# Kernel optimization log

Measured on AMD Instinct MI355X. Metric: run time of the kernel, lower is better.

## Reference

```python
import jax, jax.numpy as jnp
import numpy as np

N_E = 1024
E_DIM = 512
LEGACY_CLUSTER = 0.2
LEGACY_ENERGY = 0.2


def setup_inputs() -> dict:
    key = jax.random.key(0)
    k1, k2 = jax.random.split(key)
    B, T = 64, 512
    key_soft = jax.random.normal(k1, (B, T, E_DIM), dtype=jnp.float32)
    zero_ts_mask = jnp.zeros((B,), dtype=bool)
    # nn.Embedding(1+n_e, e_dim) initialized uniform(-1/n_e, 1/n_e)
    emb_weight = jax.random.uniform(k2, (N_E + 1, E_DIM), dtype=jnp.float32,
                                    minval=-1.0 / N_E, maxval=1.0 / N_E)
    return {"key_soft": key_soft, "zero_ts_mask": zero_ts_mask, "emb_weight": emb_weight}


def _compute_indices(d3, zero_ts_mask, n_e):
    # d3: [B, T, n_e+1] squared distances (treated as constants: torch.no_grad)
    ind0 = jnp.clip(jnp.argmin(d3[:, 0, :], axis=1), 0, n_e - 1)
    ind0 = jnp.where(zero_ts_mask, 0, ind0)

    def step(ind, d_t):
        # d_t: [B, n_e+1]; neighbor-constrained argmin: stay at ind or move to ind+1
        d_here = jnp.take_along_axis(d_t, ind[:, None], axis=1)[:, 0]
        ind_next = jnp.clip(ind + 1, 0, n_e - 1)
        d_next = jnp.take_along_axis(d_t, ind_next[:, None], axis=1)[:, 0]
        new_ind = jnp.where(d_here <= d_next, ind, ind_next)
        return new_ind, new_ind

    d_rest = jnp.swapaxes(d3[:, 1:, :], 0, 1)  # [T-1, B, n_e+1] time-major
    _, inds_rest = jax.lax.scan(step, ind0, d_rest)
    return jnp.concatenate([ind0[:, None], jnp.swapaxes(inds_rest, 0, 1)], axis=1)  # [B, T]


def reference(key_soft, zero_ts_mask, emb_weight):
    sg = jax.lax.stop_gradient
    B, T, e_dim = key_soft.shape
    n_e = emb_weight.shape[0] - 1
    ksf = key_soft.reshape(-1, e_dim)  # [B*T, e_dim]
    # squared euclidean distances to all 1+n_e codes: [B*T, n_e+1]
    d = (jnp.sum(ksf ** 2, axis=1, keepdims=True)
         + jnp.sum(emb_weight ** 2, axis=1)
         - 2.0 * jnp.einsum('bd,nd->bn', ksf, emb_weight))
    min_indices = jnp.argmin(d, axis=1)  # [B*T]
    d3 = d.reshape(B, T, n_e + 1)
    encoding_indices = _compute_indices(sg(d3), zero_ts_mask, n_e)  # [B, T]

    key_hard_here = emb_weight[encoding_indices]        # [B, T, e_dim]
    key_hard_next = emb_weight[encoding_indices + 1]    # [B, T, e_dim]
    key_min = emb_weight[min_indices].reshape(B, T, e_dim)

    key_em_here = (jnp.sum((sg(key_soft) - key_hard_here) ** 2, axis=-1)
                   + jnp.sum((key_soft - sg(key_hard_here)) ** 2, axis=-1) * LEGACY_ENERGY)
    key_em_next = (jnp.sum((sg(key_soft) - key_hard_next) ** 2, axis=-1)
                   + jnp.sum((key_soft - sg(key_hard_next)) ** 2, axis=-1) * LEGACY_ENERGY)
    key_energy_mat = key_em_next - key_em_here  # [B, T]

    ind_change = (encoding_indices[:, 1:] - encoding_indices[:, :-1]).astype(bool)
    key_energy_change = (key_energy_mat[:, 1:] - key_energy_mat[:, :-1]) * jnp.where(ind_change, 0.0, 1.0)
    eps = 1e-06 / n_e
    loss_key_energy_descent = jnp.maximum(key_energy_change + eps, 0.0).mean()

    loss_min_indices = (jnp.sum((sg(key_soft) - key_min) ** 2, axis=-1)
                        + jnp.sum((key_soft - sg(key_min)) ** 2, axis=-1) * LEGACY_CLUSTER)
    reg_persist_mat = jnp.exp(-key_em_next)
    e_normal_mat = jnp.where(key_em_here > loss_min_indices - eps,
                             key_em_here - loss_min_indices + eps,
                             key_em_here) + reg_persist_mat
    e_abnormal_mat = key_em_next + jnp.exp(-key_em_here)

    key_hard = key_soft + sg(key_hard_here - key_soft)  # straight-through
    v = jnp.max(jnp.max(encoding_indices, axis=1) - jnp.min(encoding_indices, axis=1))
    return (key_hard, encoding_indices, v, loss_key_energy_descent,
            key_energy_mat, e_normal_mat, e_abnormal_mat)
```

## Files before the change

### kernel.cpp

```cpp
#include <hip/hip_runtime.h>
#include <math.h>

typedef unsigned char u8;
typedef unsigned short u16;
typedef unsigned int u32;
typedef __attribute__((ext_vector_type(8))) short bf16x8;
typedef __attribute__((ext_vector_type(4))) float f32x4;

#define O1 16777216
#define O2 16809984
#define O3 16809985
#define O4 16809986
#define O5 16842754
#define O6 16875522

#define W_COLSQ 0
#define W_MINV  4352
#define W_MINI  2101504
#define W_SF    4198656
#define W_SL    6426880
#define W_BITS  8524032
#define W_MIDX  12718336
#define W_ENC   12849408
#define W_V     12980480
#define W_P5    12980736
#define W_EH    13000704
#define W_EL    14050304

__device__ __forceinline__ u32 cvt_pk(float lo, float hi) {
  u32 r;
  asm volatile("v_cvt_pk_bf16_f32 %0, %1, %2" : "=v"(r) : "v"(lo), "v"(hi));
  return r;
}
__device__ __forceinline__ float asf(u32 u) { return __uint_as_float(u); }

__device__ __forceinline__ void gload_lds16(const void* g, void* l) {
  __builtin_amdgcn_global_load_lds(
      (const __attribute__((address_space(1))) unsigned int*)g,
      (__attribute__((address_space(3))) unsigned int*)l, 16, 0, 0);
}

__global__ __launch_bounds__(256) void k0_colsq(const float* __restrict__ emb,
                                                float* __restrict__ colsq,
                                                u32* __restrict__ emb_hi,
                                                u32* __restrict__ emb_lo) {
  int w = threadIdx.x >> 6, lane = threadIdx.x & 63;
  int c = blockIdx.x * 4 + w;
  if (c >= 1025) return;
  const float4* e4 = (const float4*)(emb + (size_t)c * 512);
  float4 a = e4[lane * 2], b = e4[lane * 2 + 1];
  float p = a.x * a.x + a.y * a.y + a.z * a.z + a.w * a.w
          + b.x * b.x + b.y * b.y + b.z * b.z + b.w * b.w;
  #pragma unroll
  for (int off = 32; off; off >>= 1) p += __shfl_xor(p, off);
  if (lane == 0) colsq[c] = p;
  u32 h0 = cvt_pk(a.x, a.y), h1 = cvt_pk(a.z, a.w);
  u32 h2 = cvt_pk(b.x, b.y), h3 = cvt_pk(b.z, b.w);
  float l0 = a.x - asf(h0 << 16), l1 = a.y - asf(h0 & 0xFFFF0000u);
  float l2 = a.z - asf(h1 << 16), l3 = a.w - asf(h1 & 0xFFFF0000u);
  float l4 = b.x - asf(h2 << 16), l5 = b.y - asf(h2 & 0xFFFF0000u);
  float l6 = b.z - asf(h3 << 16), l7 = b.w - asf(h3 & 0xFFFF0000u);
  uint4 hv; hv.x = h0; hv.y = h1; hv.z = h2; hv.w = h3;
  uint4 lv; lv.x = cvt_pk(l0, l1); lv.y = cvt_pk(l2, l3);
  lv.z = cvt_pk(l4, l5); lv.w = cvt_pk(l6, l7);
  ((uint4*)emb_hi)[c * 64 + lane] = hv;
  ((uint4*)emb_lo)[c * 64 + lane] = lv;
}

__global__ __launch_bounds__(256) void k1_gemm(const float* __restrict__ ksf,
                                               const u32* __restrict__ emb_hi,
                                               const u32* __restrict__ emb_lo,
                                               const float* __restrict__ colsq,
                                               float* __restrict__ minv, int* __restrict__ mini,
                                               float* __restrict__ sF, float* __restrict__ sL,
                                               u8* __restrict__ bits) {
  __shared__ float smemf[16384];
  char* smc = (char*)smemf;
  const int tid = threadIdx.x, bid = blockIdx.x;
  const int g = bid >> 6;
  const int cbk = (bid >> 3) & 7;
  const int rb = g * 8 + (bid & 7);
  const int r0 = rb * 128, c0 = cbk * 128;
  const int lane = tid & 63, w = tid >> 6;
  const int wr = w >> 1, wc = w & 1;
  const int q = lane >> 4, li = lane & 15;

  int offS[4], baseA[4];
  #pragma unroll
  for (int i = 0; i < 4; i++) {
    int p = tid + (i << 8);
    int row = p >> 3, q8 = p & 7;
    offS[i] = row * 64 + ((q8 * 8) ^ (((row >> 1) & 3) << 4));
    baseA[i] = (r0 + row) * 128 + q8;
  }
  const int rowj0 = w * 32 + (lane >> 2), rowj1 = rowj0 + 16;
  const int qb = lane & 3;
  const int offB0 = (c0 + rowj0) * 1024 + ((qb ^ ((rowj0 >> 1) & 3)) << 4);
  const int offB1 = (c0 + rowj1) * 1024 + ((qb ^ ((rowj1 >> 1) & 3)) << 4);
  const char* ebh = (const char*)emb_hi;
  const char* ebl = (const char*)emb_lo;

  int foA[4], foB[4];
  #pragma unroll
  for (int m = 0; m < 4; m++) {
    int row = wr * 64 + m * 16 + li;
    foA[m] = row * 64 + ((q * 16) ^ (((row >> 1) & 3) << 4));
    int col = wc * 64 + m * 16 + li;
    foB[m] = col * 64 + ((q * 16) ^ (((col >> 1) & 3) << 4));
  }

  f32x4 acc[4][4];
  #pragma unroll
  for (int m = 0; m < 4; m++)
    #pragma unroll
    for (int n = 0; n < 4; n++) acc[m][n] = (f32x4){0.f, 0.f, 0.f, 0.f};

  const float4* A4 = (const float4*)ksf;
  float4 ra[4];

  auto stageB = [&](int bb, int t1) {
    int ko = t1 * 64;
    char* d0 = smc + bb + 16384 + w * 2048;
    gload_lds16(ebh + offB0 + ko, d0);
    gload_lds16(ebh + offB1 + ko, d0 + 1024);
    gload_lds16(ebl + offB0 + ko, d0 + 8192);
    gload_lds16(ebl + offB1 + ko, d0 + 9216);
  };
  auto stageA = [&](int bb) {
    #pragma unroll
    for (int i = 0; i < 4; i++) {
      float4 v = ra[i];
      u32 w0 = cvt_pk(v.x, v.y), w1 = cvt_pk(v.z, v.w);
      float lx = v.x - asf(w0 << 16);
      float ly = v.y - asf(w0 & 0xFFFF0000u);
      float lz = v.z - asf(w1 << 16);
      float lw = v.w - asf(w1 & 0xFFFF0000u);
      u32 m0 = cvt_pk(lx, ly), m1 = cvt_pk(lz, lw);
      uint2 hv; hv.x = w0; hv.y = w1;
      uint2 lv; lv.x = m0; lv.y = m1;
      *(uint2*)(smc + bb + offS[i]) = hv;
      *(uint2*)(smc + bb + 8192 + offS[i]) = lv;
    }
  };
  auto mfma_phase = [&](int bb) {
    bf16x8 fA[4], fB[4], fX[4];
    #pragma unroll
    for (int m = 0; m < 4; m++) fA[m] = *(const bf16x8*)(smc + bb + foA[m]);
    #pragma unroll
    for (int n = 0; n < 4; n++) fB[n] = *(const bf16x8*)(smc + bb + 16384 + foB[n]);
    #pragma unroll
    for (int m = 0; m < 4; m++)
      #pragma unroll
      for (int n = 0; n < 4; n++)
        acc[m][n] = __builtin_amdgcn_mfma_f32_16x16x32_bf16(fA[m], fB[n], acc[m][n], 0, 0, 0);
    #pragma unroll
    for (int n = 0; n < 4; n++) fX[n] = *(const bf16x8*)(smc + bb + 24576 + foB[n]);
    #pragma unroll
    for (int m = 0; m < 4; m++)
      #pragma unroll
      for (int n = 0; n < 4; n++)
        acc[m][n] = __builtin_amdgcn_mfma_f32_16x16x32_bf16(fA[m], fX[n], acc[m][n], 0, 0, 0);
    #pragma unroll
    for (int m = 0; m < 4; m++) fA[m] = *(const bf16x8*)(smc + bb + 8192 + foA[m]);
    #pragma unroll
    for (int m = 0; m < 4; m++)
      #pragma unroll
      for (int n = 0; n < 4; n++)
        acc[m][n] = __builtin_amdgcn_mfma_f32_16x16x32_bf16(fA[m], fB[n], acc[m][n], 0, 0, 0);
  };

  #pragma unroll
  for (int i = 0; i < 4; i++) ra[i] = A4[baseA[i]];
  stageB(0, 0);
  stageA(0);
  #pragma unroll
  for (int i = 0; i < 4; i++) ra[i] = A4[baseA[i] + 8];
  __syncthreads();

  #pragma unroll 1
  for (int tp = 0; tp < 8; tp++) {
    int t = tp * 2;
    {
      stageB(32768, t + 1);
      stageA(32768);
      if (t < 14) {
        #pragma unroll
        for (int i = 0; i < 4; i++) ra[i] = A4[baseA[i] + (t + 2) * 8];
      }
      __builtin_amdgcn_s_setprio(1);
      mfma_phase(0);
      __builtin_amdgcn_s_setprio(0);
      __syncthreads();
    }
    {
      int t1 = t + 1;
      if (t1 < 15) {
        stageB(0, t1 + 1);
        stageA(0);
        if (t1 < 14) {
          #pragma unroll
          for (int i = 0; i < 4; i++) ra[i] = A4[baseA[i] + (t1 + 2) * 8];
        }
      }
      __builtin_amdgcn_s_setprio(1);
      mfma_phase(32768);
      __builtin_amdgcn_s_setprio(0);
      __syncthreads();
    }
  }

  float cs4[4];
  #pragma unroll
  for (int n = 0; n < 4; n++) cs4[n] = colsq[c0 + wc * 64 + n * 16 + li];
  const int ct = tid & 15, rt = tid >> 4;
  for (int h = 0; h < 2; h++) {
    __syncthreads();
    if (wr == h) {
      #pragma unroll
      for (int m = 0; m < 4; m++) {
        int rl = m * 16 + q * 4;
        #pragma unroll
        for (int n = 0; n < 4; n++) {
          int cl = wc * 64 + n * 16 + li;
          #pragma unroll
          for (int r = 0; r < 4; r++)
            smemf[(rl + r) * 132 + cl] = fmaf(acc[m][n][r], -2.0f, cs4[n]);
        }
      }
    }
    __syncthreads();
    #pragma unroll
    for (int j = 0; j < 4; j++) {
      int rl = rt * 4 + j;
      int rowg = r0 + h * 64 + rl;
      const float* sp = &smemf[rl * 132 + ct * 8];
      float4 sa = *(const float4*)sp, sb = *(const float4*)(sp + 4);
      float s[8] = {sa.x, sa.y, sa.z, sa.w, sb.x, sb.y, sb.z, sb.w};
      float sn0 = __shfl_down(s[0], 1, 16);
      u32 bv = 0;
      #pragma unroll
      for (int i = 0; i < 7; i++) bv |= (s[i] <= s[i + 1]) ? (1u << i) : 0u;
      bv |= (s[7] <= sn0) ? 0x80u : 0u;
      bits[rowg * 128 + cbk * 16 + ct] = (u8)bv;
      int cbase = c0 + ct * 8;
      float mv = s[0]; int mi = cbase;
      #pragma unroll
      for (int i = 1; i < 8; i++) if (s[i] < mv) { mv = s[i]; mi = cbase + i; }
      #pragma unroll
      for (int d = 4; d >= 1; d >>= 1) {
        float ov = __shfl_xor(mv, d, 8);
        int oi = __shfl_xor(mi, d, 8);
        if (ov < mv || (ov == mv && oi < mi)) { mv = ov; mi = oi; }
      }
      int sb64 = cbk * 2 + (ct >> 3);
      if ((ct & 7) == 0) {
        minv[rowg * 16 + sb64] = mv;
        mini[rowg * 16 + sb64] = mi;
        sF[rowg * 17 + sb64] = s[0];
      }
      if ((ct & 7) == 7) sL[rowg * 16 + sb64] = s[7];
    }
  }
}

__global__ __launch_bounds__(256) void k1b_col1024(const float* __restrict__ ksf,
                                                   const float* __restrict__ emb,
                                                   const float* __restrict__ colsq,
                                                   float* __restrict__ sF) {
  int wid = threadIdx.x >> 6, lane = threadIdx.x & 63;
  int row = blockIdx.x * 4 + wid;
  const float4* ks4 = (const float4*)(ksf + (size_t)row * 512);
  const float4* e4 = (const float4*)(emb + (size_t)1024 * 512);
  float4 a = ks4[lane * 2], b = ks4[lane * 2 + 1];
  float4 ea = e4[lane * 2], eb = e4[lane * 2 + 1];
  float p = a.x * ea.x + a.y * ea.y + a.z * ea.z + a.w * ea.w
          + b.x * eb.x + b.y * eb.y + b.z * eb.z + b.w * eb.w;
  #pragma unroll
  for (int off = 32; off; off >>= 1) p += __shfl_xor(p, off);
  if (lane == 0) sF[row * 17 + 16] = fmaf(p, -2.0f, colsq[1024]);
}

__global__ __launch_bounds__(256) void k2_combine(const float* __restrict__ minv,
                                                  const int* __restrict__ mini,
                                                  const float* __restrict__ sF,
                                                  const float* __restrict__ sL,
                                                  u8* __restrict__ bits,
                                                  int* __restrict__ midx, int* __restrict__ vslot) {
  int row = blockIdx.x * 256 + threadIdx.x;
  if (blockIdx.x == 0 && threadIdx.x == 0) *vslot = 0;
  float bv = minv[row * 16];
  int bi = mini[row * 16];
  #pragma unroll
  for (int cb = 1; cb < 16; cb++) {
    float v = minv[row * 16 + cb];
    int ii = mini[row * 16 + cb];
    if (v < bv) { bv = v; bi = ii; }
  }
  float s1024 = sF[row * 17 + 16];
  if (s1024 < bv) { bv = s1024; bi = 1024; }
  midx[row] = bi;
  #pragma unroll
  for (int cb = 0; cb < 16; cb++) {
    float nb = (cb < 15) ? sF[row * 17 + cb + 1] : s1024;
    u8 bit = (sL[row * 16 + cb] <= nb) ? (u8)0x80 : (u8)0;
    int a = row * 128 + cb * 8 + 7;
    bits[a] = (u8)((bits[a] & 0x7F) | bit);
  }
}

__global__ __launch_bounds__(256) void k3_scan(const u8* __restrict__ bits,
                                               const int* __restrict__ midx,
                                               const u8* __restrict__ mask,
                                               int* __restrict__ enc, int* __restrict__ vslot) {
  __shared__ u32 bl[256 * 32];
  __shared__ int el[512];
  int b = blockIdx.x, tid = threadIdx.x, lane = tid & 63;
  const u32* bw = (const u32*)bits;
  for (int phase = 0; phase < 2; phase++) {
    int t0 = 1 + phase * 256;
    int nt = phase ? 255 : 256;
    __syncthreads();
    for (int ww = tid; ww < nt * 32; ww += 256)
      bl[ww] = bw[(size_t)(b * 512 + t0) * 32 + ww];
    __syncthreads();
    if (tid < 64) {
      int ind;
      if (phase == 0) {
        int mi = midx[b * 512];
        ind = mi < 1023 ? mi : 1023;
        if (ind < 0) ind = 0;
        if (mask[b]) ind = 0;
        if (lane == 0) el[0] = ind;
      } else {
        ind = el[256];
      }
      int done = 0;
      while (done < nt) {
        int W = nt - done; if (W > 64) W = 64;
        int i0 = ind;
        int p = i0 + lane;
        u32 mlo = 0xFFFFFFFFu, mhi = 0xFFFFFFFFu;
        if (p < 1023) {
          int base = done * 32 + (p >> 5);
          int sh = p & 31;
          mlo = 0; mhi = 0;
          #pragma unroll
          for (int s = 0; s < 32; s++)
            mlo |= ((bl[base + s * 32] >> sh) & 1u) << s;
          #pragma unroll
          for (int s = 0; s < 32; s++)
            mhi |= ((bl[base + (s + 32) * 32] >> sh) & 1u) << s;
        }
        int rel = 0, myel = 0;
        #pragma unroll
        for (int s = 0; s < 64; s++) {
          u32 wv = (s < 32) ? __builtin_amdgcn_readlane(mlo, rel)
                            : __builtin_amdgcn_readlane(mhi, rel);
          rel += 1 - (int)((wv >> (s & 31)) & 1u);
          if (lane == s) myel = i0 + rel;
        }
        if (lane < W) el[t0 + done + lane] = myel;
        ind = (int)__builtin_amdgcn_readlane((u32)myel, (u32)(W - 1));
        done += W;
      }
    }
  }
  __syncthreads();
  for (int t = tid; t < 512; t += 256) enc[b * 512 + t] = el[t];
  if (tid == 0) atomicMax(vslot, el[511] - el[0]);
}

__global__ __launch_bounds__(256) void k4_energy(const float* __restrict__ ksf,
                                                 const float* __restrict__ emb,
                                                 const int* __restrict__ enc_a,
                                                 const int* __restrict__ midx,
                                                 float* __restrict__ out) {
  int wid = threadIdx.x >> 6, lane = threadIdx.x & 63;
  int row = blockIdx.x * 4 + wid;
  int eh = enc_a[row];
  int mi = midx[row];
  eh = (eh < 0) ? 0 : (eh > 1023 ? 1023 : eh);
  mi = (mi < 0) ? 0 : (mi > 1024 ? 1024 : mi);
  const float4* ks4 = (const float4*)(ksf + (size_t)row * 512);
  const float4* h4 = (const float4*)(emb + (size_t)eh * 512);
  const float4* n4 = (const float4*)(emb + (size_t)(eh + 1) * 512);
  const float4* m4 = (const float4*)(emb + (size_t)mi * 512);
  float ph = 0.f, pn = 0.f, pm = 0.f;
  float4 kh[2];
  #pragma unroll
  for (int u = 0; u < 2; u++) {
    float4 k = ks4[lane * 2 + u], h = h4[lane * 2 + u], n = n4[lane * 2 + u], m = m4[lane * 2 + u];
    float d;
    d = k.x - h.x; ph = fmaf(d, d, ph);
    d = k.y - h.y; ph = fmaf(d, d, ph);
    d = k.z - h.z; ph = fmaf(d, d, ph);
    d = k.w - h.w; ph = fmaf(d, d, ph);
    d = k.x - n.x; pn = fmaf(d, d, pn);
    d = k.y - n.y; pn = fmaf(d, d, pn);
    d = k.z - n.z; pn = fmaf(d, d, pn);
    d = k.w - n.w; pn = fmaf(d, d, pn);
    d = k.x - m.x; pm = fmaf(d, d, pm);
    d = k.y - m.y; pm = fmaf(d, d, pm);
    d = k.z - m.z; pm = fmaf(d, d, pm);
    d = k.w - m.w; pm = fmaf(d, d, pm);
    kh[u].x = k.x + (h.x - k.x);
    kh[u].y = k.y + (h.y - k.y);
    kh[u].z = k.z + (h.z - k.z);
    kh[u].w = k.w + (h.w - k.w);
  }
  #pragma unroll
  for (int off = 32; off; off >>= 1) {
    ph += __shfl_xor(ph, off);
    pn += __shfl_xor(pn, off);
    pm += __shfl_xor(pm, off);
  }
  float4* o0 = (float4*)out;
  o0[(size_t)row * 128 + lane * 2] = kh[0];
  o0[(size_t)row * 128 + lane * 2 + 1] = kh[1];
  if (lane == 0) {
    const float epsN = 9.765625e-10f;
    float kemh = ph + ph * 0.2f;
    float kemn = pn + pn * 0.2f;
    float lmin = pm + pm * 0.2f;
    float lminu = fminf(lmin, kemh);
    out[O1 + row] = (float)eh;
    out[O4 + row] = kemn - kemh;
    float env = (kemh > lminu - epsN) ? ((kemh - lminu) + epsN) : kemh;
    out[O5 + row] = env + expf(-kemn);
    out[O6 + row] = kemn + expf(-kemh);
  }
}

__global__ __launch_bounds__(256) void k5a_part(const float* __restrict__ kem,
                                                const int* __restrict__ enc,
                                                float* __restrict__ partial) {
  __shared__ float red[256];
  int tid = threadIdx.x;
  int i = blockIdx.x * 256 + tid;
  const float epsN = 9.765625e-10f;
  float p = 0.f;
  if (i & 511) {
    float diff = kem[i] - kem[i - 1];
    if (enc[i] != enc[i - 1]) diff = 0.f;
    float v = diff + epsN;
    p = (v > 0.f) ? v : 0.f;
  }
  red[tid] = p;
  __syncthreads();
  #pragma unroll
  for (int s = 128; s; s >>= 1) {
    if (tid < s) red[tid] += red[tid + s];
    __syncthreads();
  }
  if (tid == 0) partial[blockIdx.x] = red[0];
}

__global__ __launch_bounds__(64) void k5b_final(const float* __restrict__ partial,
                                                const int* __restrict__ vslot,
                                                float* __restrict__ out) {
  int lane = threadIdx.x;
  float p = partial[lane] + partial[lane + 64];
  #pragma unroll
  for (int off = 32; off; off >>= 1) p += __shfl_xor(p, off);
  if (lane == 0) {
    out[O3] = p / 32704.0f;
    out[O2] = (float)(*vslot);
  }
}

extern "C" void kernel_launch(void* const* d_in, const int* in_sizes, int n_in,
                              void* d_out, int out_size, void* d_ws, size_t ws_size,
                              hipStream_t stream) {
  const float* ksf = (const float*)d_in[0];
  const u8* mask = (const u8*)d_in[1];
  const float* emb = (const float*)d_in[2];
  float* out = (float*)d_out;
  char* ws = (char*)d_ws;
  float* colsq = (float*)(ws + W_COLSQ);
  float* minv = (float*)(ws + W_MINV);
  int* mini = (int*)(ws + W_MINI);
  float* sF = (float*)(ws + W_SF);
  float* sL = (float*)(ws + W_SL);
  u8* bits = (u8*)(ws + W_BITS);
  int* midx = (int*)(ws + W_MIDX);
  int* enc = (int*)(ws + W_ENC);
  int* vslot = (int*)(ws + W_V);
  u32* emb_hi = (u32*)(ws + W_EH);
  u32* emb_lo = (u32*)(ws + W_EL);
  float* part5 = (float*)(ws + W_P5);

  hipLaunchKernelGGL(k0_colsq, dim3(257), dim3(256), 0, stream, emb, colsq, emb_hi, emb_lo);
  hipLaunchKernelGGL(k1_gemm, dim3(2048), dim3(256), 0, stream, ksf, emb_hi, emb_lo, colsq,
                     minv, mini, sF, sL, bits);
  hipLaunchKernelGGL(k1b_col1024, dim3(8192), dim3(256), 0, stream, ksf, emb, colsq, sF);
  hipLaunchKernelGGL(k2_combine, dim3(128), dim3(256), 0, stream, minv, mini, sF, sL,
                     bits, midx, vslot);
  hipLaunchKernelGGL(k3_scan, dim3(64), dim3(256), 0, stream, bits, midx, mask, enc, vslot);
  hipLaunchKernelGGL(k4_energy, dim3(8192), dim3(256), 0, stream, ksf, emb, enc, midx, out);
  hipLaunchKernelGGL(k5a_part, dim3(128), dim3(256), 0, stream, out + O4, enc, part5);
  hipLaunchKernelGGL(k5b_final, dim3(1), dim3(64), 0, stream, part5, vslot, out);
}
```

Before: 193.0 us.

## Load codebook B fragments directly from global into registers, shrink LDS for occupancy

Codebook hi/lo bf16 fragments are no longer staged into LDS through global_load_lds. Each wave now reads its own B fragments straight from global (L2-resident) memory into registers right before the MFMA phase. This halves the shared-memory footprint, and the launch bounds now request 3 blocks per CU to raise occupancy. The cost is that B loads are issued without prefetch and are duplicated across the two row-waves, so global latency sits directly ahead of the MFMAs.

```diff
diff --git a/kernel.cpp b/kernel.cpp
--- a/kernel.cpp
+++ b/kernel.cpp
@@ -33,12 +33,6 @@
   return r;
 }
 __device__ __forceinline__ float asf(u32 u) { return __uint_as_float(u); }
-
-__device__ __forceinline__ void gload_lds16(const void* g, void* l) {
-  __builtin_amdgcn_global_load_lds(
-      (const __attribute__((address_space(1))) unsigned int*)g,
-      (__attribute__((address_space(3))) unsigned int*)l, 16, 0, 0);
-}
 
 __global__ __launch_bounds__(256) void k0_colsq(const float* __restrict__ emb,
                                                 float* __restrict__ colsq,
@@ -67,14 +61,14 @@
   ((uint4*)emb_lo)[c * 64 + lane] = lv;
 }
 
-__global__ __launch_bounds__(256) void k1_gemm(const float* __restrict__ ksf,
-                                               const u32* __restrict__ emb_hi,
-                                               const u32* __restrict__ emb_lo,
-                                               const float* __restrict__ colsq,
-                                               float* __restrict__ minv, int* __restrict__ mini,
-                                               float* __restrict__ sF, float* __restrict__ sL,
-                                               u8* __restrict__ bits) {
-  __shared__ float smemf[16384];
+__global__ __launch_bounds__(256, 3) void k1_gemm(const float* __restrict__ ksf,
+                                                  const u32* __restrict__ emb_hi,
+                                                  const u32* __restrict__ emb_lo,
+                                                  const float* __restrict__ colsq,
+                                                  float* __restrict__ minv, int* __restrict__ mini,
+                                                  float* __restrict__ sF, float* __restrict__ sL,
+                                                  u8* __restrict__ bits) {
+  __shared__ float smemf[8448];
   char* smc = (char*)smemf;
   const int tid = threadIdx.x, bid = blockIdx.x;
   const int g = bid >> 6;
@@ -93,20 +87,20 @@
     offS[i] = row * 64 + ((q8 * 8) ^ (((row >> 1) & 3) << 4));
     baseA[i] = (r0 + row) * 128 + q8;
   }
-  const int rowj0 = w * 32 + (lane >> 2), rowj1 = rowj0 + 16;
-  const int qb = lane & 3;
-  const int offB0 = (c0 + rowj0) * 1024 + ((qb ^ ((rowj0 >> 1) & 3)) << 4);
-  const int offB1 = (c0 + rowj1) * 1024 + ((qb ^ ((rowj1 >> 1) & 3)) << 4);
+  int baseB[4];
+  #pragma unroll
+  for (int n = 0; n < 4; n++) {
+    int col = c0 + wc * 64 + n * 16 + li;
+    baseB[n] = col * 1024 + q * 16;
+  }
   const char* ebh = (const char*)emb_hi;
   const char* ebl = (const char*)emb_lo;
 
-  int foA[4], foB[4];
+  int foA[4];
   #pragma unroll
   for (int m = 0; m < 4; m++) {
     int row = wr * 64 + m * 16 + li;
     foA[m] = row * 64 + ((q * 16) ^ (((row >> 1) & 3) << 4));
-    int col = wc * 64 + m * 16 + li;
-    foB[m] = col * 64 + ((q * 16) ^ (((col >> 1) & 3) << 4));
   }
 
   f32x4 acc[4][4];
@@ -118,14 +112,6 @@
   const float4* A4 = (const float4*)ksf;
   float4 ra[4];
 
-  auto stageB = [&](int bb, int t1) {
-    int ko = t1 * 64;
-    char* d0 = smc + bb + 16384 + w * 2048;
-    gload_lds16(ebh + offB0 + ko, d0);
-    gload_lds16(ebh + offB1 + ko, d0 + 1024);
-    gload_lds16(ebl + offB0 + ko, d0 + 8192);
-    gload_lds16(ebl + offB1 + ko, d0 + 9216);
-  };
   auto stageA = [&](int bb) {
     #pragma unroll
     for (int i = 0; i < 4; i++) {
@@ -142,36 +128,31 @@
       *(uint2*)(smc + bb + 8192 + offS[i]) = lv;
     }
   };
-  auto mfma_phase = [&](int bb) {
-    bf16x8 fA[4], fB[4], fX[4];
+  auto mfma_phase = [&](int bb, const bf16x8* fB, const bf16x8* fX) {
+    bf16x8 fA[4], fL[4];
     #pragma unroll
     for (int m = 0; m < 4; m++) fA[m] = *(const bf16x8*)(smc + bb + foA[m]);
-    #pragma unroll
-    for (int n = 0; n < 4; n++) fB[n] = *(const bf16x8*)(smc + bb + 16384 + foB[n]);
     #pragma unroll
     for (int m = 0; m < 4; m++)
       #pragma unroll
       for (int n = 0; n < 4; n++)
         acc[m][n] = __builtin_amdgcn_mfma_f32_16x16x32_bf16(fA[m], fB[n], acc[m][n], 0, 0, 0);
     #pragma unroll
-    for (int n = 0; n < 4; n++) fX[n] = *(const bf16x8*)(smc + bb + 24576 + foB[n]);
-    #pragma unroll
     for (int m = 0; m < 4; m++)
       #pragma unroll
       for (int n = 0; n < 4; n++)
         acc[m][n] = __builtin_amdgcn_mfma_f32_16x16x32_bf16(fA[m], fX[n], acc[m][n], 0, 0, 0);
     #pragma unroll
-    for (int m = 0; m < 4; m++) fA[m] = *(const bf16x8*)(smc + bb + 8192 + foA[m]);
+    for (int m = 0; m < 4; m++) fL[m] = *(const bf16x8*)(smc + bb + 8192 + foA[m]);
     #pragma unroll
     for (int m = 0; m < 4; m++)
       #pragma unroll
       for (int n = 0; n < 4; n++)
-        acc[m][n] = __builtin_amdgcn_mfma_f32_16x16x32_bf16(fA[m], fB[n], acc[m][n], 0, 0, 0);
+        acc[m][n] = __builtin_amdgcn_mfma_f32_16x16x32_bf16(fL[m], fB[n], acc[m][n], 0, 0, 0);
   };
 
   #pragma unroll
   for (int i = 0; i < 4; i++) ra[i] = A4[baseA[i]];
-  stageB(0, 0);
   stageA(0);
   #pragma unroll
   for (int i = 0; i < 4; i++) ra[i] = A4[baseA[i] + 8];
@@ -181,21 +162,31 @@
   for (int tp = 0; tp < 8; tp++) {
     int t = tp * 2;
     {
-      stageB(32768, t + 1);
-      stageA(32768);
+      bf16x8 fB[4], fX[4];
+      #pragma unroll
+      for (int n = 0; n < 4; n++) {
+        fB[n] = *(const bf16x8*)(ebh + baseB[n] + t * 64);
+        fX[n] = *(const bf16x8*)(ebl + baseB[n] + t * 64);
+      }
+      stageA(16384);
       if (t < 14) {
         #pragma unroll
         for (int i = 0; i < 4; i++) ra[i] = A4[baseA[i] + (t + 2) * 8];
       }
       __builtin_amdgcn_s_setprio(1);
-      mfma_phase(0);
+      mfma_phase(0, fB, fX);
       __builtin_amdgcn_s_setprio(0);
       __syncthreads();
     }
     {
       int t1 = t + 1;
+      bf16x8 fB[4], fX[4];
+      #pragma unroll
+      for (int n = 0; n < 4; n++) {
+        fB[n] = *(const bf16x8*)(ebh + baseB[n] + t1 * 64);
+        fX[n] = *(const bf16x8*)(ebl + baseB[n] + t1 * 64);
+      }
       if (t1 < 15) {
-        stageB(0, t1 + 1);
         stageA(0);
         if (t1 < 14) {
           #pragma unroll
@@ -203,7 +194,7 @@
         }
       }
       __builtin_amdgcn_s_setprio(1);
-      mfma_phase(32768);
+      mfma_phase(16384, fB, fX);
       __builtin_amdgcn_s_setprio(0);
       __syncthreads();
     }
```

Result: slower. 340.6 us (+76.4%).

## Load emb low-part fragments directly from global in MFMA-ready layout, shrink LDS

Applied to the files above, without the earlier changes.

The k0 kernel now writes the low-bf16 part of the embedding in a pre-swizzled layout that matches the MFMA B-fragment order. The GEMM kernel reads these fragments straight from global memory into registers instead of staging them through LDS. This cuts LDS usage from 64KB to 48KB per block, which may raise occupancy and reduce LDS traffic. In exchange, the MFMA phase now waits on global load latency, and the 1025th code row's low part is no longer written.

```diff
diff --git a/kernel.cpp b/kernel.cpp
--- a/kernel.cpp
+++ b/kernel.cpp
@@ -27,6 +27,8 @@
 #define W_EH    13000704
 #define W_EL    14050304
 
+#define BUFST 24576
+
 __device__ __forceinline__ u32 cvt_pk(float lo, float hi) {
   u32 r;
   asm volatile("v_cvt_pk_bf16_f32 %0, %1, %2" : "=v"(r) : "v"(lo), "v"(hi));
@@ -64,7 +66,11 @@
   uint4 lv; lv.x = cvt_pk(l0, l1); lv.y = cvt_pk(l2, l3);
   lv.z = cvt_pk(l4, l5); lv.w = cvt_pk(l6, l7);
   ((uint4*)emb_hi)[c * 64 + lane] = hv;
-  ((uint4*)emb_lo)[c * 64 + lane] = lv;
+  if (c < 1024) {
+    int t = lane >> 2, qq = lane & 3;
+    int idx = (t * 16 + (c >> 6)) * 256 + ((c >> 4) & 3) * 64 + qq * 16 + (c & 15);
+    ((uint4*)emb_lo)[idx] = lv;
+  }
 }
 
 __global__ __launch_bounds__(256) void k1_gemm(const float* __restrict__ ksf,
@@ -74,7 +80,7 @@
                                                float* __restrict__ minv, int* __restrict__ mini,
                                                float* __restrict__ sF, float* __restrict__ sL,
                                                u8* __restrict__ bits) {
-  __shared__ float smemf[16384];
+  __shared__ float smemf[12288];
   char* smc = (char*)smemf;
   const int tid = threadIdx.x, bid = blockIdx.x;
   const int g = bid >> 6;
@@ -98,7 +104,8 @@
   const int offB0 = (c0 + rowj0) * 1024 + ((qb ^ ((rowj0 >> 1) & 3)) << 4);
   const int offB1 = (c0 + rowj1) * 1024 + ((qb ^ ((rowj1 >> 1) & 3)) << 4);
   const char* ebh = (const char*)emb_hi;
-  const char* ebl = (const char*)emb_lo;
+  const int baseL = (cbk * 2 + wc) * 256 + lane;
+  const uint4* Bl4 = (const uint4*)emb_lo;
 
   int foA[4], foB[4];
   #pragma unroll
@@ -123,8 +130,6 @@
     char* d0 = smc + bb + 16384 + w * 2048;
     gload_lds16(ebh + offB0 + ko, d0);
     gload_lds16(ebh + offB1 + ko, d0 + 1024);
-    gload_lds16(ebl + offB0 + ko, d0 + 8192);
-    gload_lds16(ebl + offB1 + ko, d0 + 9216);
   };
   auto stageA = [&](int bb) {
     #pragma unroll
@@ -142,8 +147,11 @@
       *(uint2*)(smc + bb + 8192 + offS[i]) = lv;
     }
   };
-  auto mfma_phase = [&](int bb) {
-    bf16x8 fA[4], fB[4], fX[4];
+  auto mfma_phase = [&](int bb, int t) {
+    bf16x8 gX[4];
+    #pragma unroll
+    for (int n = 0; n < 4; n++) gX[n] = *(const bf16x8*)&Bl4[t * 4096 + baseL + n * 64];
+    bf16x8 fA[4], fB[4], fL[4];
     #pragma unroll
     for (int m = 0; m < 4; m++) fA[m] = *(const bf16x8*)(smc + bb + foA[m]);
     #pragma unroll
@@ -154,19 +162,17 @@
       for (int n = 0; n < 4; n++)
         acc[m][n] = __builtin_amdgcn_mfma_f32_16x16x32_bf16(fA[m], fB[n], acc[m][n], 0, 0, 0);
     #pragma unroll
-    for (int n = 0; n < 4; n++) fX[n] = *(const bf16x8*)(smc + bb + 24576 + foB[n]);
-    #pragma unroll
     for (int m = 0; m < 4; m++)
       #pragma unroll
       for (int n = 0; n < 4; n++)
-        acc[m][n] = __builtin_amdgcn_mfma_f32_16x16x32_bf16(fA[m], fX[n], acc[m][n], 0, 0, 0);
-    #pragma unroll
-    for (int m = 0; m < 4; m++) fA[m] = *(const bf16x8*)(smc + bb + 8192 + foA[m]);
+        acc[m][n] = __builtin_amdgcn_mfma_f32_16x16x32_bf16(fA[m], gX[n], acc[m][n], 0, 0, 0);
+    #pragma unroll
+    for (int m = 0; m < 4; m++) fL[m] = *(const bf16x8*)(smc + bb + 8192 + foA[m]);
     #pragma unroll
     for (int m = 0; m < 4; m++)
       #pragma unroll
       for (int n = 0; n < 4; n++)
-        acc[m][n] = __builtin_amdgcn_mfma_f32_16x16x32_bf16(fA[m], fB[n], acc[m][n], 0, 0, 0);
+        acc[m][n] = __builtin_amdgcn_mfma_f32_16x16x32_bf16(fL[m], fB[n], acc[m][n], 0, 0, 0);
   };
 
   #pragma unroll
@@ -181,14 +187,14 @@
   for (int tp = 0; tp < 8; tp++) {
     int t = tp * 2;
     {
-      stageB(32768, t + 1);
-      stageA(32768);
+      stageB(BUFST, t + 1);
+      stageA(BUFST);
       if (t < 14) {
         #pragma unroll
         for (int i = 0; i < 4; i++) ra[i] = A4[baseA[i] + (t + 2) * 8];
       }
       __builtin_amdgcn_s_setprio(1);
-      mfma_phase(0);
+      mfma_phase(0, t);
       __builtin_amdgcn_s_setprio(0);
       __syncthreads();
     }
@@ -203,7 +209,7 @@
         }
       }
       __builtin_amdgcn_s_setprio(1);
-      mfma_phase(32768);
+      mfma_phase(BUFST, t1);
       __builtin_amdgcn_s_setprio(0);
       __syncthreads();
     }
```

Result: no change. 191.3 us (-0.9%).

## Fuse code-1024 distance column into GEMM blocks, drop separate kernel

Applied to the files above, without the earlier changes.

The extra distance column for code 1024 was computed by a separate kernel that re-read all of key_soft from global memory. Blocks handling the last column tile now hold the code-1024 row in registers and add extra split-bf16 MFMAs against the already-staged A fragments, writing sF column 16 directly. This removes one launch and a full pass over the 64MB input. In exchange, those blocks do extra MFMAs and register loads and become slightly imbalanced, and precision changes from fp32 FMA to a 3-term bf16 split.

```diff
diff --git a/kernel.cpp b/kernel.cpp
--- a/kernel.cpp
+++ b/kernel.cpp
@@ -81,6 +81,7 @@
   const int cbk = (bid >> 3) & 7;
   const int rb = g * 8 + (bid & 7);
   const int r0 = rb * 128, c0 = cbk * 128;
+  const bool cb7 = (cbk == 7);
   const int lane = tid & 63, w = tid >> 6;
   const int wr = w >> 1, wc = w & 1;
   const int q = lane >> 4, li = lane & 15;
@@ -99,6 +100,8 @@
   const int offB1 = (c0 + rowj1) * 1024 + ((qb ^ ((rowj1 >> 1) & 3)) << 4);
   const char* ebh = (const char*)emb_hi;
   const char* ebl = (const char*)emb_lo;
+  const char* e1024h = ebh + 1048576 + q * 16;
+  const char* e1024l = ebl + 1048576 + q * 16;
 
   int foA[4], foB[4];
   #pragma unroll
@@ -109,14 +112,18 @@
     foB[m] = col * 64 + ((q * 16) ^ (((col >> 1) & 3) << 4));
   }
 
-  f32x4 acc[4][4];
-  #pragma unroll
-  for (int m = 0; m < 4; m++)
+  f32x4 acc[4][4], acce[4];
+  #pragma unroll
+  for (int m = 0; m < 4; m++) {
+    acce[m] = (f32x4){0.f, 0.f, 0.f, 0.f};
     #pragma unroll
     for (int n = 0; n < 4; n++) acc[m][n] = (f32x4){0.f, 0.f, 0.f, 0.f};
+  }
 
   const float4* A4 = (const float4*)ksf;
   float4 ra[4];
+  bf16x8 reAh = {0,0,0,0,0,0,0,0}, reAl = {0,0,0,0,0,0,0,0};
+  bf16x8 reBh = {0,0,0,0,0,0,0,0}, reBl = {0,0,0,0,0,0,0,0};
 
   auto stageB = [&](int bb, int t1) {
     int ko = t1 * 64;
@@ -142,7 +149,7 @@
       *(uint2*)(smc + bb + 8192 + offS[i]) = lv;
     }
   };
-  auto mfma_phase = [&](int bb) {
+  auto mfma_phase = [&](int bb, bf16x8 feh, bf16x8 fel) {
     bf16x8 fA[4], fB[4], fX[4];
     #pragma unroll
     for (int m = 0; m < 4; m++) fA[m] = *(const bf16x8*)(smc + bb + foA[m]);
@@ -160,6 +167,14 @@
       #pragma unroll
       for (int n = 0; n < 4; n++)
         acc[m][n] = __builtin_amdgcn_mfma_f32_16x16x32_bf16(fA[m], fX[n], acc[m][n], 0, 0, 0);
+    if (cb7) {
+      #pragma unroll
+      for (int m = 0; m < 4; m++)
+        acce[m] = __builtin_amdgcn_mfma_f32_16x16x32_bf16(fA[m], feh, acce[m], 0, 0, 0);
+      #pragma unroll
+      for (int m = 0; m < 4; m++)
+        acce[m] = __builtin_amdgcn_mfma_f32_16x16x32_bf16(fA[m], fel, acce[m], 0, 0, 0);
+    }
     #pragma unroll
     for (int m = 0; m < 4; m++) fA[m] = *(const bf16x8*)(smc + bb + 8192 + foA[m]);
     #pragma unroll
@@ -167,10 +182,16 @@
       #pragma unroll
       for (int n = 0; n < 4; n++)
         acc[m][n] = __builtin_amdgcn_mfma_f32_16x16x32_bf16(fA[m], fB[n], acc[m][n], 0, 0, 0);
+    if (cb7) {
+      #pragma unroll
+      for (int m = 0; m < 4; m++)
+        acce[m] = __builtin_amdgcn_mfma_f32_16x16x32_bf16(fA[m], feh, acce[m], 0, 0, 0);
+    }
   };
 
   #pragma unroll
   for (int i = 0; i < 4; i++) ra[i] = A4[baseA[i]];
+  if (cb7) { reAh = *(const bf16x8*)(e1024h); reAl = *(const bf16x8*)(e1024l); }
   stageB(0, 0);
   stageA(0);
   #pragma unroll
@@ -183,12 +204,16 @@
     {
       stageB(32768, t + 1);
       stageA(32768);
+      if (cb7) {
+        reBh = *(const bf16x8*)(e1024h + (t + 1) * 64);
+        reBl = *(const bf16x8*)(e1024l + (t + 1) * 64);
+      }
       if (t < 14) {
         #pragma unroll
         for (int i = 0; i < 4; i++) ra[i] = A4[baseA[i] + (t + 2) * 8];
       }
       __builtin_amdgcn_s_setprio(1);
-      mfma_phase(0);
+      mfma_phase(0, reAh, reAl);
       __builtin_amdgcn_s_setprio(0);
       __syncthreads();
     }
@@ -197,16 +222,31 @@
       if (t1 < 15) {
         stageB(0, t1 + 1);
         stageA(0);
+        if (cb7) {
+          reAh = *(const bf16x8*)(e1024h + (t1 + 1) * 64);
+          reAl = *(const bf16x8*)(e1024l + (t1 + 1) * 64);
+        }
         if (t1 < 14) {
           #pragma unroll
           for (int i = 0; i < 4; i++) ra[i] = A4[baseA[i] + (t1 + 2) * 8];
         }
       }
       __builtin_amdgcn_s_setprio(1);
-      mfma_phase(32768);
+      mfma_phase(32768, reBh, reBl);
       __builtin_amdgcn_s_setprio(0);
       __syncthreads();
     }
+  }
+
+  if (cb7 && wc == 0 && li == 0) {
+    float cq = colsq[1024];
+    #pragma unroll
+    for (int m = 0; m < 4; m++)
+      #pragma unroll
+      for (int r = 0; r < 4; r++) {
+        int rowg = r0 + wr * 64 + m * 16 + q * 4 + r;
+        sF[rowg * 17 + 16] = fmaf(acce[m][r], -2.0f, cq);
+      }
   }
 
   float cs4[4];
@@ -261,23 +301,6 @@
       if ((ct & 7) == 7) sL[rowg * 16 + sb64] = s[7];
     }
   }
-}
-
-__global__ __launch_bounds__(256) void k1b_col1024(const float* __restrict__ ksf,
-                                                   const float* __restrict__ emb,
-                                                   const float* __restrict__ colsq,
-                                                   float* __restrict__ sF) {
-  int wid = threadIdx.x >> 6, lane = threadIdx.x & 63;
-  int row = blockIdx.x * 4 + wid;
-  const float4* ks4 = (const float4*)(ksf + (size_t)row * 512);
-  const float4* e4 = (const float4*)(emb + (size_t)1024 * 512);
-  float4 a = ks4[lane * 2], b = ks4[lane * 2 + 1];
-  float4 ea = e4[lane * 2], eb = e4[lane * 2 + 1];
-  float p = a.x * ea.x + a.y * ea.y + a.z * ea.z + a.w * ea.w
-          + b.x * eb.x + b.y * eb.y + b.z * eb.z + b.w * eb.w;
-  #pragma unroll
-  for (int off = 32; off; off >>= 1) p += __shfl_xor(p, off);
-  if (lane == 0) sF[row * 17 + 16] = fmaf(p, -2.0f, colsq[1024]);
 }
 
 __global__ __launch_bounds__(256) void k2_combine(const float* __restrict__ minv,
@@ -492,7 +515,6 @@
   hipLaunchKernelGGL(k0_colsq, dim3(257), dim3(256), 0, stream, emb, colsq, emb_hi, emb_lo);
   hipLaunchKernelGGL(k1_gemm, dim3(2048), dim3(256), 0, stream, ksf, emb_hi, emb_lo, colsq,
                      minv, mini, sF, sL, bits);
-  hipLaunchKernelGGL(k1b_col1024, dim3(8192), dim3(256), 0, stream, ksf, emb, colsq, sF);
   hipLaunchKernelGGL(k2_combine, dim3(128), dim3(256), 0, stream, minv, mini, sF, sL,
                      bits, midx, vslot);
   hipLaunchKernelGGL(k3_scan, dim3(64), dim3(256), 0, stream, bits, midx, mask, enc, vslot);
```

Measured after the change: 191.6 us, median of 2. Within noise of the previous version (-0.8%).
